# Kernel tuning notes

Measured on AMD Instinct MI355X. Metric: run time of the kernel, lower is better.

The kernel has to match this reference:

```python
import jax, jax.numpy as jnp
import numpy as np

STRIDE = 32
ANCHOR_SCALES = (16, 32, 64)
RATIOS = (0.5, 1.0, 2.0)
BASE_SIZE = 16
A = 9                    # base_anchors
PRE_NMS_TOP_N = 6000
POST_NMS_TOP_N = 1000
NMS_THRESH = 0.7
MIN_SIZE = 16.0


def _base_anchors():
    w = h = float(BASE_SIZE)
    cx = cy = (BASE_SIZE - 1) * 0.5
    out = []
    for r in RATIOS:
        ws = np.round(np.sqrt(w * h / r))
        hs = np.round(ws * r)
        for s in ANCHOR_SCALES:
            W_, H_ = ws * s, hs * s
            out.append([cx - 0.5 * (W_ - 1), cy - 0.5 * (H_ - 1),
                        cx + 0.5 * (W_ - 1), cy + 0.5 * (H_ - 1)])
    return np.asarray(out, dtype=np.float32)  # [9,4]


def _conv(x, w, b, padding):
    y = jax.lax.conv_general_dilated(x, w, (1, 1), padding,
                                     dimension_numbers=('NCHW', 'OIHW', 'NCHW'))
    return y + b[None, :, None, None]


def reference(features, rpn_w, rpn_b, cls_w, cls_b, box_w, box_b, image_height, image_width):
    H, W = features.shape[2], features.shape[3]
    x = jax.nn.relu(_conv(features, rpn_w, rpn_b, 'SAME'))
    cls_score = _conv(x, cls_w, cls_b, 'VALID')           # [1,2A,H,W]
    cls_prob = jax.nn.softmax(cls_score, axis=1)           # nn.Softmax2d: softmax over all 2A channels
    bbox_pred = _conv(x, box_w, box_b, 'VALID')            # [1,4A,H,W]

    scores = cls_prob[0, A:].transpose(1, 2, 0).reshape(-1)       # fg scores [H*W*A]
    deltas = bbox_pred[0].transpose(1, 2, 0).reshape(-1, 4)        # [H*W*A,4]

    base = jnp.asarray(_base_anchors())
    sx = jnp.arange(W, dtype=jnp.float32) * STRIDE
    sy = jnp.arange(H, dtype=jnp.float32) * STRIDE
    sxx, syy = jnp.meshgrid(sx, sy)                                # [H,W]
    shifts = jnp.stack([sxx, syy, sxx, syy], axis=-1).reshape(-1, 4)
    anchors = (shifts[:, None, :] + base[None, :, :]).reshape(-1, 4)

    # bbox_transform_inv decode
    wa = anchors[:, 2] - anchors[:, 0] + 1.0
    ha = anchors[:, 3] - anchors[:, 1] + 1.0
    cxa = anchors[:, 0] + 0.5 * (wa - 1.0)
    cya = anchors[:, 1] + 0.5 * (ha - 1.0)
    cx = deltas[:, 0] * wa + cxa
    cy = deltas[:, 1] * ha + cya
    pw = wa * jnp.exp(deltas[:, 2])
    ph = ha * jnp.exp(deltas[:, 3])
    x1 = jnp.clip(cx - 0.5 * pw, 0.0, image_width - 1.0)
    y1 = jnp.clip(cy - 0.5 * ph, 0.0, image_height - 1.0)
    x2 = jnp.clip(cx + 0.5 * pw, 0.0, image_width - 1.0)
    y2 = jnp.clip(cy + 0.5 * ph, 0.0, image_height - 1.0)
    boxes = jnp.stack([x1, y1, x2, y2], axis=-1)

    valid0 = ((x2 - x1 + 1.0) >= MIN_SIZE) & ((y2 - y1 + 1.0) >= MIN_SIZE)
    scores = jnp.where(valid0, scores, -jnp.inf)

    top_scores, top_idx = jax.lax.top_k(scores, PRE_NMS_TOP_N)
    tb = boxes[top_idx]                                             # [P,4]
    tx1, ty1, tx2, ty2 = tb[:, 0], tb[:, 1], tb[:, 2], tb[:, 3]
    areas = (tx2 - tx1 + 1.0) * (ty2 - ty1 + 1.0)
    xx1 = jnp.maximum(tx1[:, None], tx1[None, :])
    yy1 = jnp.maximum(ty1[:, None], ty1[None, :])
    xx2 = jnp.minimum(tx2[:, None], tx2[None, :])
    yy2 = jnp.minimum(ty2[:, None], ty2[None, :])
    inter = jnp.maximum(xx2 - xx1 + 1.0, 0.0) * jnp.maximum(yy2 - yy1 + 1.0, 0.0)
    iou = inter / (areas[:, None] + areas[None, :] - inter)         # [P,P]

    def step(state, _):
        alive, = (state,) if not isinstance(state, tuple) else (None,)
        return state, None

    def nms_step(state, _):
        alive, sel_list = state
        s = jnp.where(alive, top_scores, -jnp.inf)
        j = jnp.argmax(s)
        ok = s[j] > -jnp.inf
        alive = alive & (jnp.take(iou, j, axis=0) <= NMS_THRESH)    # suppresses j too (iou=1)
        return (alive, sel_list), (j.astype(jnp.int32), ok)

    alive0 = jnp.isfinite(top_scores)
    (_, _), (sel, selv) = jax.lax.scan(nms_step, (alive0, 0),
                                       jnp.arange(POST_NMS_TOP_N), length=POST_NMS_TOP_N)

    out_boxes = tb[sel] * selv[:, None].astype(tb.dtype)            # zero-pad invalid slots
    rois = jnp.concatenate([jnp.zeros((POST_NMS_TOP_N, 1), tb.dtype), out_boxes], axis=1)
    return rois                                                     # [POST_NMS_TOP_N, 5]


def setup_inputs() -> dict:
    key = jax.random.key(0)
    ks = jax.random.split(key, 4)
    features = jax.random.normal(ks[0], (1, 256, 128, 128), dtype=jnp.float32)
    rpn_w = 0.01 * jax.random.normal(ks[1], (256, 256, 3, 3), dtype=jnp.float32)
    rpn_b = jnp.zeros((256,), jnp.float32)
    cls_w = 0.01 * jax.random.normal(ks[2], (18, 256, 1, 1), dtype=jnp.float32)
    cls_b = jnp.zeros((18,), jnp.float32)
    box_w = 0.01 * jax.random.normal(ks[3], (36, 256, 1, 1), dtype=jnp.float32)
    box_b = jnp.zeros((36,), jnp.float32)
    return {'features': features, 'rpn_w': rpn_w, 'rpn_b': rpn_b,
            'cls_w': cls_w, 'cls_b': cls_b, 'box_w': box_w, 'box_b': box_b,
            'image_height': 4096, 'image_width': 4096}
```

## Files before the change

kernel.cpp:

```cpp
#include <hip/hip_runtime.h>
#include <stdint.h>
#include <math.h>

typedef unsigned long long u64;
typedef unsigned int u32;
typedef float float4a __attribute__((ext_vector_type(4), aligned(4)));

static const size_t OFF_CTL   = 0;
static const size_t OFF_HIST  = 1024;
static const size_t OFF_DOTS  = 1049600;
static const size_t OFF_WCV   = 4588544;
static const size_t OFF_XD    = 6947840;
static const size_t OFF_BOX   = 23725056;
static const size_t OFF_KEYS  = 26084352;
static const size_t OFF_CKEY  = 27264000;
static const size_t OFF_CIDX  = 27313152;
static const size_t OFF_TB    = 27337728;
static const size_t OFF_TSC   = 27433728;
static const size_t OFF_ALIVE = 27458048;
static const size_t OFF_MASK  = 27459072;
static const size_t OFF_FPAD  = 32067584;

__device__ __forceinline__ float exp_xla(float x) {
    float m = floorf(__fmaf_rn(x, 1.44269504088896341f, 0.5f));
    float r = __fmaf_rn(m, -0.693359375f, x);
    r = __fmaf_rn(m, 2.12194440e-4f, r);
    float r2 = r * r;
    float p = 1.9875691500e-4f;
    p = __fmaf_rn(p, r, 1.3981999507e-3f);
    p = __fmaf_rn(p, r, 8.3334519073e-3f);
    p = __fmaf_rn(p, r, 4.1665795894e-2f);
    p = __fmaf_rn(p, r, 1.6666665459e-1f);
    p = __fmaf_rn(p, r, 5.0000001201e-1f);
    p = __fmaf_rn(p, r2, r);
    p = __fadd_rn(p, 1.0f);
    int mi = (int)m;
    return p * __int_as_float((mi + 127) << 23);
}

__device__ __forceinline__ void gload_lds16(const void* g, void* l) {
    __builtin_amdgcn_global_load_lds(
        (const __attribute__((address_space(1))) void*)g,
        (__attribute__((address_space(3))) void*)l, 16, 0, 0);
}

__global__ void prep_wcv(const float* __restrict__ rpn_w, float* __restrict__ wcv) {
    int t = blockIdx.x * 256 + threadIdx.x;
    if (t >= 589824) return;
    int tap = t / 65536, rem = t % 65536, ic = rem / 256, oc = rem % 256;
    wcv[t] = rpn_w[oc * 2304 + ic * 9 + tap];
}

__global__ void prep_pad(const float* __restrict__ feat, float* __restrict__ featP) {
    int t = blockIdx.x * 256 + threadIdx.x;
    if (t >= 256 * 130 * 132) return;
    int ic = t / 17160, rem = t % 17160, y = rem / 132, x = rem % 132;
    int sy = y - 1, sx = x - 1;
    float v = 0.f;
    if (sy >= 0 && sy < 128 && sx >= 0 && sx < 128)
        v = feat[ic * 16384 + sy * 128 + sx];
    featP[t] = v;
}

__global__ __launch_bounds__(256, 2) void conv3x3(const float* __restrict__ featP,
                                                  const float* __restrict__ wcv,
                                                  const float* __restrict__ rpn_b,
                                                  float* __restrict__ xd) {
    __shared__ float sW[8192];
    const int band = blockIdx.x & 7;
    const int slot = blockIdx.x >> 3;
    const int tx = slot & 7, ocb = slot >> 3;
    const int oc0 = ocb * 32;
    const int tid = threadIdx.x;
    const int wid = tid >> 6;
    const int lane = tid & 63;
    const int py = lane >> 2, px0 = (lane & 3) * 4;
    const int gy = band * 16 + py, gx0 = tx * 16 + px0;
    const int ocB = oc0 + wid * 8;
    float acc[4][8];
#pragma unroll
    for (int p = 0; p < 4; ++p)
#pragma unroll
        for (int o = 0; o < 8; ++o) acc[p][o] = 0.f;
#pragma unroll
    for (int tap = 0; tap < 9; ++tap) {
        __syncthreads();
        for (int idx = tid; idx < 8192; idx += 256)
            sW[idx] = wcv[tap * 65536 + (idx >> 5) * 256 + oc0 + (idx & 31)];
        __syncthreads();
        const float* fp = featP + (size_t)(gy + tap / 3) * 132 + (gx0 + tap % 3);
        const float* wl = sW + wid * 8;
#pragma unroll 4
        for (int ic = 0; ic < 256; ++ic) {
            float4a fA = *(const float4a*)(fp + (size_t)ic * 17160);
            float4a w0 = *(const float4a*)(wl + ic * 32);
            float4a w1 = *(const float4a*)(wl + ic * 32 + 4);
#pragma unroll
            for (int p = 0; p < 4; ++p) {
#pragma unroll
                for (int o = 0; o < 4; ++o)
                    acc[p][o] = __fmaf_rn(fA[p], w0[o], acc[p][o]);
#pragma unroll
                for (int o = 0; o < 4; ++o)
                    acc[p][4 + o] = __fmaf_rn(fA[p], w1[o], acc[p][4 + o]);
            }
        }
    }
#pragma unroll
    for (int p = 0; p < 4; ++p) {
        float* op = xd + (size_t)(gy * 128 + gx0 + p) * 256 + ocB;
#pragma unroll
        for (int o = 0; o < 8; ++o) {
            float v = __fadd_rn(acc[p][o], rpn_b[ocB + o]);
            op[o] = v > 0.f ? v : 0.f;
        }
    }
}

__global__ __launch_bounds__(256, 1) void heads_seq(const float* __restrict__ xd,
                                                    const float* __restrict__ cls_w,
                                                    const float* __restrict__ box_w,
                                                    float* __restrict__ dots) {
    __shared__ float sX[4][260];
    const int tid = threadIdx.x;
    const int pix0 = blockIdx.x * 4;
    for (int idx = tid; idx < 1024; idx += 256)
        sX[idx >> 8][idx & 255] = xd[(size_t)(pix0 + (idx >> 8)) * 256 + (idx & 255)];
    __syncthreads();
    if (tid < 216) {
        const int pl = tid / 54, o = tid % 54;
        const float* wr = (o < 18) ? (cls_w + o * 256) : (box_w + (o - 18) * 256);
        const float4* x4 = (const float4*)&sX[pl][0];
        const float4* w4 = (const float4*)wr;
        float acc = 0.f;
        for (int q = 0; q < 64; ++q) {
            float4 xv = x4[q];
            float4 wv = w4[q];
            acc = __fmaf_rn(xv.x, wv.x, acc);
            acc = __fmaf_rn(xv.y, wv.y, acc);
            acc = __fmaf_rn(xv.z, wv.z, acc);
            acc = __fmaf_rn(xv.w, wv.w, acc);
        }
        dots[(size_t)(pix0 + pl) * 54 + o] = acc;
    }
}

__global__ __launch_bounds__(256, 1) void decode(const float* __restrict__ dots,
                                                 const float* __restrict__ cls_b,
                                                 const float* __restrict__ box_b,
                                                 float4* __restrict__ boxes,
                                                 u64* __restrict__ keys) {
    const int pix = blockIdx.x * 256 + threadIdx.x;
    if (pix >= 16384) return;
    const float* dt = dots + (size_t)pix * 54;
    float d[54];
#pragma unroll
    for (int i = 0; i < 54; ++i)
        d[i] = __fadd_rn(dt[i], (i < 18 ? cls_b[i] : box_b[i - 18]));
    float m = d[0];
#pragma unroll
    for (int i = 1; i < 18; ++i) m = fmaxf(m, d[i]);
    float e[18];
#pragma unroll
    for (int i = 0; i < 18; ++i) e[i] = exp_xla(__fsub_rn(d[i], m));
    float s = e[0];
#pragma unroll
    for (int i = 1; i < 18; ++i) s = __fadd_rn(s, e[i]);
    const int y = pix >> 7, x = pix & 127;
    const float shx = (float)(x * 32), shy = (float)(y * 32);
    const float AW[9] = {368.f, 736.f, 1472.f, 256.f, 512.f, 1024.f, 176.f, 352.f, 704.f};
    const float AH[9] = {192.f, 384.f, 768.f, 256.f, 512.f, 1024.f, 352.f, 704.f, 1408.f};
#pragma unroll
    for (int a = 0; a < 9; ++a) {
        float score = e[9 + a] / s;
        float wa = AW[a], ha = AH[a];
        float cxa = __fadd_rn(shx, 7.5f), cya = __fadd_rn(shy, 7.5f);
        float dx = d[18 + 4 * a], dyy = d[19 + 4 * a];
        float dw = d[20 + 4 * a], dh = d[21 + 4 * a];
        float cx = __fadd_rn(__fmul_rn(dx, wa), cxa);
        float cy = __fadd_rn(__fmul_rn(dyy, ha), cya);
        float pw = __fmul_rn(wa, exp_xla(dw));
        float ph = __fmul_rn(ha, exp_xla(dh));
        float hx = __fmul_rn(0.5f, pw), hy = __fmul_rn(0.5f, ph);
        float x1 = fminf(fmaxf(__fsub_rn(cx, hx), 0.f), 4095.f);
        float y1 = fminf(fmaxf(__fsub_rn(cy, hy), 0.f), 4095.f);
        float x2 = fminf(fmaxf(__fadd_rn(cx, hx), 0.f), 4095.f);
        float y2 = fminf(fmaxf(__fadd_rn(cy, hy), 0.f), 4095.f);
        float vw = __fadd_rn(__fsub_rn(x2, x1), 1.0f);
        float vh = __fadd_rn(__fsub_rn(y2, y1), 1.0f);
        bool valid = (vw >= 16.0f) && (vh >= 16.0f);
        int i = pix * 9 + a;
        boxes[i] = make_float4(x1, y1, x2, y2);
        u64 k;
        if (valid) {
            u32 b = __float_as_uint(score);
            k = ((u64)(u32)~(b | 0x80000000u) << 32) | (u32)i;
        } else {
            k = (0xFFFFFFFFULL << 32) | (u32)i;
        }
        keys[i] = k;
    }
}

__global__ __launch_bounds__(256) void hist8(const u64* __restrict__ keys,
                                             u32* __restrict__ ghist,
                                             const u64* __restrict__ pfx, int pass) {
    __shared__ u32 lh[256];
    lh[threadIdx.x] = 0;
    __syncthreads();
    const u64 pref = *pfx;
    const int shift = 56 - 8 * pass;
    for (int i = blockIdx.x * 256 + threadIdx.x; i < 147456; i += 64 * 256) {
        u64 k = keys[i];
        bool match = (pass == 0) || ((k >> (shift + 8)) == pref);
        if (match) atomicAdd(&lh[(u32)(k >> shift) & 0xFFu], 1u);
    }
    __syncthreads();
    if (lh[threadIdx.x]) atomicAdd(&ghist[threadIdx.x], lh[threadIdx.x]);
}

__global__ __launch_bounds__(256) void scan8(const u32* __restrict__ ghist,
                                             u64* pfx, u32* tgt, int pass) {
    __shared__ u32 h[256];
    __shared__ u32 incl[256];
    const int t = threadIdx.x;
    u32 target = (pass == 0) ? 6000u : *tgt;
    u64 p0 = (pass == 0) ? 0ULL : *pfx;
    h[t] = ghist[t];
    incl[t] = h[t];
    __syncthreads();
    for (int off = 1; off < 256; off <<= 1) {
        u32 v = (t >= off) ? incl[t - off] : 0u;
        __syncthreads();
        incl[t] += v;
        __syncthreads();
    }
    u32 before = incl[t] - h[t];
    if (before < target && target <= incl[t]) {
        *pfx = (p0 << 8) | (u64)t;
        *tgt = target - before;
    }
}

__global__ void compact(const u64* __restrict__ keys, const u64* __restrict__ kstar,
                        u32* count, u64* __restrict__ ckey, u32* __restrict__ cidx) {
    int i = blockIdx.x * 256 + threadIdx.x;
    if (i >= 147456) return;
    u64 k = keys[i];
    if (k <= *kstar) {
        u32 pos = atomicAdd(count, 1u);
        if (pos < 6144) { ckey[pos] = k; cidx[pos] = (u32)(k & 0xFFFFFFFFu); }
    }
}

__global__ __launch_bounds__(256) void rank_scatter(const u64* __restrict__ ckey,
                                                    const u32* __restrict__ cidx,
                                                    const u32* __restrict__ count,
                                                    const float4* __restrict__ boxes,
                                                    float4* __restrict__ tb,
                                                    float* __restrict__ tsc) {
    __shared__ u64 LK[6144];
    int N = (int)*count; if (N > 6144) N = 6144;
    for (int i = threadIdx.x; i < N; i += 256) LK[i] = ckey[i];
    __syncthreads();
    int e = blockIdx.x * 256 + threadIdx.x;
    if (e >= N) return;
    u64 myK = LK[e];
    u32 myI = cidx[e];
    int rank = 0;
    for (int c = 0; c < N; ++c) rank += (LK[c] < myK);
    if (rank < 6000) {
        tb[rank] = boxes[myI];
        u32 hi = (u32)(myK >> 32);
        tsc[rank] = (hi == 0xFFFFFFFFu) ? -__builtin_inff()
                                        : __uint_as_float(~hi & 0x7FFFFFFFu);
    }
}

__global__ void alive_init(const float* __restrict__ tsc, u64* __restrict__ alive0) {
    int r = blockIdx.x * 256 + threadIdx.x;
    bool a = false;
    if (r < 6000) a = tsc[r] > -__builtin_inff();
    u64 b = __ballot(a);
    if ((threadIdx.x & 63) == 0) alive0[r >> 6] = b;
}

__global__ __launch_bounds__(256) void nms_mask(const float4* __restrict__ tb,
                                                u64* __restrict__ mask) {
    int tid = blockIdx.x * 256 + threadIdx.x;
    if (tid >= 6000 * 94) return;
    int j = tid / 94, w = tid % 94;
    float4 bj = tb[j];
    float arJ = __fmul_rn(__fadd_rn(__fsub_rn(bj.z, bj.x), 1.0f),
                          __fadd_rn(__fsub_rn(bj.w, bj.y), 1.0f));
    u64 m = 0;
    int base = w * 64;
#pragma unroll 4
    for (int b = 0; b < 64; ++b) {
        int i = base + b;
        if (i >= 6000) break;
        float4 bi = tb[i];
        float arI = __fmul_rn(__fadd_rn(__fsub_rn(bi.z, bi.x), 1.0f),
                              __fadd_rn(__fsub_rn(bi.w, bi.y), 1.0f));
        float xx1 = fmaxf(bj.x, bi.x), yy1 = fmaxf(bj.y, bi.y);
        float xx2 = fminf(bj.z, bi.z), yy2 = fminf(bj.w, bi.w);
        float ww = fmaxf(__fadd_rn(__fsub_rn(xx2, xx1), 1.0f), 0.0f);
        float hh = fmaxf(__fadd_rn(__fsub_rn(yy2, yy1), 1.0f), 0.0f);
        float inter = __fmul_rn(ww, hh);
        float uni = __fsub_rn(__fadd_rn(arJ, arI), inter);
        float iou = inter / uni;
        if (iou > 0.7f) m |= (1ULL << b);
    }
    mask[(size_t)j * 96 + w] = m;
}

__global__ __launch_bounds__(64, 1) void nms_seq(const u64* __restrict__ alive0,
                                                 const u64* __restrict__ mask,
                                                 const float4* __restrict__ tb,
                                                 float* __restrict__ out) {
    __shared__ __align__(16) u64 lwin[2][64 * 96];
    __shared__ u32 sel[1000];
    const int lane = threadIdx.x;
    u64 wl = alive0[lane];
    u64 wh = (lane < 30) ? alive0[64 + lane] : 0ULL;
    int base = -1000000;
    int pbase = -1;
    int cur = 0;
    int k = 0;
    for (; k < 1000; ++k) {
        int j;
        {
            u64 blo = __ballot(wl != 0ULL);
            if (blo) {
                int l = __ffsll((long long)blo) - 1;
                u32 a = __builtin_amdgcn_readlane((u32)wl, l);
                u32 b = __builtin_amdgcn_readlane((u32)(wl >> 32), l);
                u64 w = ((u64)b << 32) | (u64)a;
                j = l * 64 + __ffsll((long long)w) - 1;
            } else {
                u64 bhi = __ballot(wh != 0ULL);
                if (!bhi) break;
                int l = __ffsll((long long)bhi) - 1;
                u32 a = __builtin_amdgcn_readlane((u32)wh, l);
                u32 b = __builtin_amdgcn_readlane((u32)(wh >> 32), l);
                u64 w = ((u64)b << 32) | (u64)a;
                j = (64 + l) * 64 + __ffsll((long long)w) - 1;
            }
        }
        if (lane == 0) sel[k] = (u32)j;
        if (j >= base + 64) {
            if (pbase >= 0 && j < pbase + 64) {
                asm volatile("s_waitcnt vmcnt(0)" ::: "memory");
                cur ^= 1;
                base = pbase;
            } else {
                int js = (j > 5936) ? 5936 : j;
                asm volatile("s_waitcnt vmcnt(0)" ::: "memory");
                const char* gsrc = (const char*)mask + (size_t)js * 768 + (size_t)lane * 16;
                char* ldst = (char*)&lwin[cur][0];
#pragma unroll
                for (int i = 0; i < 48; ++i)
                    gload_lds16(gsrc + (size_t)i * 1024, ldst + i * 1024);
                base = js;
                asm volatile("s_waitcnt vmcnt(0)" ::: "memory");
            }
            pbase = -1;
            if (base + 64 < 6000) {
                int ps = (base + 64 > 5936) ? 5936 : (base + 64);
                const char* gs2 = (const char*)mask + (size_t)ps * 768 + (size_t)lane * 16;
                char* ld2 = (char*)&lwin[cur ^ 1][0];
#pragma unroll
                for (int i = 0; i < 48; ++i)
                    gload_lds16(gs2 + (size_t)i * 1024, ld2 + i * 1024);
                pbase = ps;
            }
        }
        const int s = j - base;
        u64 rl = lwin[cur][(size_t)s * 96 + lane];
        u64 rh = (lane < 30) ? lwin[cur][(size_t)s * 96 + 64 + lane] : 0ULL;
        wl &= ~rl;
        if (lane < 30) wh &= ~rh;
    }
    __syncthreads();
    for (int r = lane; r < k; r += 64) {
        int j = (int)sel[r];
        float4 bj = tb[j];
        out[r * 5 + 1] = bj.x;
        out[r * 5 + 2] = bj.y;
        out[r * 5 + 3] = bj.z;
        out[r * 5 + 4] = bj.w;
    }
}

extern "C" void kernel_launch(void* const* d_in, const int* in_sizes, int n_in,
                              void* d_out, int out_size, void* d_ws, size_t ws_size,
                              hipStream_t stream) {
    const float *feat = nullptr, *rpn_w = nullptr, *rpn_b = nullptr;
    const float *cls_w = nullptr, *cls_b = nullptr, *box_w = nullptr, *box_b = nullptr;
    for (int i = 0; i < n_in; ++i) {
        switch (in_sizes[i]) {
            case 4194304: feat  = (const float*)d_in[i]; break;
            case 589824:  rpn_w = (const float*)d_in[i]; break;
            case 256:     rpn_b = (const float*)d_in[i]; break;
            case 4608:    cls_w = (const float*)d_in[i]; break;
            case 18:      cls_b = (const float*)d_in[i]; break;
            case 9216:    box_w = (const float*)d_in[i]; break;
            case 36:      box_b = (const float*)d_in[i]; break;
            default: break;
        }
    }

    char* w = (char*)d_ws;
    u64* pfx       = (u64*)(w + OFF_CTL);
    u32* tgt       = (u32*)(w + OFF_CTL + 8);
    u32* ctlCount  = (u32*)(w + OFF_CTL + 12);
    u32* hist      = (u32*)(w + OFF_HIST);
    float* dots    = (float*)(w + OFF_DOTS);
    float* wcv     = (float*)(w + OFF_WCV);
    float* xd      = (float*)(w + OFF_XD);
    float4* boxes  = (float4*)(w + OFF_BOX);
    u64* keys      = (u64*)(w + OFF_KEYS);
    u64* ckey      = (u64*)(w + OFF_CKEY);
    u32* cidx      = (u32*)(w + OFF_CIDX);
    float4* tb     = (float4*)(w + OFF_TB);
    float* tsc     = (float*)(w + OFF_TSC);
    u64* alive0    = (u64*)(w + OFF_ALIVE);
    u64* mask      = (u64*)(w + OFF_MASK);
    float* featP   = (float*)(w + OFF_FPAD);

    hipMemsetAsync(d_ws, 0, OFF_HIST + 8 * 256 * 4, stream);
    hipMemsetAsync(d_out, 0, (size_t)out_size * sizeof(float), stream);

    prep_wcv<<<2304, 256, 0, stream>>>(rpn_w, wcv);
    prep_pad<<<17160, 256, 0, stream>>>(feat, featP);
    conv3x3<<<512, 256, 0, stream>>>(featP, wcv, rpn_b, xd);
    heads_seq<<<4096, 256, 0, stream>>>(xd, cls_w, box_w, dots);
    decode<<<64, 256, 0, stream>>>(dots, cls_b, box_b, boxes, keys);
    for (int p = 0; p < 8; ++p) {
        hist8<<<64, 256, 0, stream>>>(keys, hist + p * 256, pfx, p);
        scan8<<<1, 256, 0, stream>>>(hist + p * 256, pfx, tgt, p);
    }
    compact<<<576, 256, 0, stream>>>(keys, pfx, ctlCount, ckey, cidx);
    rank_scatter<<<24, 256, 0, stream>>>(ckey, cidx, ctlCount, boxes, tb, tsc);
    alive_init<<<24, 256, 0, stream>>>(tsc, alive0);
    nms_mask<<<2204, 256, 0, stream>>>(tb, mask);
    nms_seq<<<1, 64, 0, stream>>>(alive0, mask, tb, (float*)d_out);
}
```

Measured before the change: 912.4 us.

## Fuse histogram and scan via last-block pattern; pad NMS mask rows for vector LDS reads

Merges each radix-select histogram pass with its prefix scan into one kernel, where the last block to finish (found with an atomic counter) does the scan. This cuts eight kernel launches from the select loop. It also pads the NMS mask rows from 96 to 128 words, interleaved so each lane reads its low and high words with one 16-byte LDS load in the serial NMS loop. The cost is more mask traffic per window, the mask buffer now sharing the padded-feature region, and a reliance on threadfence ordering in the fused kernel.

```diff
diff --git a/kernel.cpp b/kernel.cpp
--- a/kernel.cpp
+++ b/kernel.cpp
@@ -5,6 +5,7 @@
 typedef unsigned long long u64;
 typedef unsigned int u32;
 typedef float float4a __attribute__((ext_vector_type(4), aligned(4)));
+typedef unsigned long long u64x2 __attribute__((ext_vector_type(2), aligned(16)));
 
 static const size_t OFF_CTL   = 0;
 static const size_t OFF_HIST  = 1024;
@@ -18,8 +19,8 @@
 static const size_t OFF_TB    = 27337728;
 static const size_t OFF_TSC   = 27433728;
 static const size_t OFF_ALIVE = 27458048;
-static const size_t OFF_MASK  = 27459072;
 static const size_t OFF_FPAD  = 32067584;
+static const size_t OFF_MASKP = OFF_FPAD;
 
 __device__ __forceinline__ float exp_xla(float x) {
     float m = floorf(__fmaf_rn(x, 1.44269504088896341f, 0.5f));
@@ -202,32 +203,39 @@
     }
 }
 
-__global__ __launch_bounds__(256) void hist8(const u64* __restrict__ keys,
-                                             u32* __restrict__ ghist,
-                                             const u64* __restrict__ pfx, int pass) {
+__global__ __launch_bounds__(256) void hist_scan(const u64* __restrict__ keys,
+                                                 u32* __restrict__ ghist,
+                                                 u64* pfx, u32* tgt,
+                                                 u32* done, int pass) {
     __shared__ u32 lh[256];
-    lh[threadIdx.x] = 0;
+    __shared__ u32 lastFlag;
+    __shared__ u32 h[256];
+    __shared__ u32 incl[256];
+    const int t = threadIdx.x;
+    lh[t] = 0;
+    if (t == 0) lastFlag = 0;
     __syncthreads();
     const u64 pref = *pfx;
+    const u32 target0 = (pass == 0) ? 6000u : *tgt;
     const int shift = 56 - 8 * pass;
-    for (int i = blockIdx.x * 256 + threadIdx.x; i < 147456; i += 64 * 256) {
+    for (int i = blockIdx.x * 256 + t; i < 147456; i += 64 * 256) {
         u64 k = keys[i];
         bool match = (pass == 0) || ((k >> (shift + 8)) == pref);
         if (match) atomicAdd(&lh[(u32)(k >> shift) & 0xFFu], 1u);
     }
     __syncthreads();
-    if (lh[threadIdx.x]) atomicAdd(&ghist[threadIdx.x], lh[threadIdx.x]);
-}
-
-__global__ __launch_bounds__(256) void scan8(const u32* __restrict__ ghist,
-                                             u64* pfx, u32* tgt, int pass) {
-    __shared__ u32 h[256];
-    __shared__ u32 incl[256];
-    const int t = threadIdx.x;
-    u32 target = (pass == 0) ? 6000u : *tgt;
-    u64 p0 = (pass == 0) ? 0ULL : *pfx;
-    h[t] = ghist[t];
-    incl[t] = h[t];
+    if (lh[t]) atomicAdd(&ghist[t], lh[t]);
+    __threadfence();
+    __syncthreads();
+    if (t == 0) {
+        u32 prev = atomicAdd(done, 1u);
+        if (prev == 63) lastFlag = 1;
+    }
+    __syncthreads();
+    if (!lastFlag) return;
+    u32 hv = atomicAdd(&ghist[t], 0u);
+    h[t] = hv;
+    incl[t] = hv;
     __syncthreads();
     for (int off = 1; off < 256; off <<= 1) {
         u32 v = (t >= off) ? incl[t - off] : 0u;
@@ -235,10 +243,11 @@
         incl[t] += v;
         __syncthreads();
     }
+    u64 p0 = (pass == 0) ? 0ULL : pref;
     u32 before = incl[t] - h[t];
-    if (before < target && target <= incl[t]) {
+    if (before < target0 && target0 <= incl[t]) {
         *pfx = (p0 << 8) | (u64)t;
-        *tgt = target - before;
+        *tgt = target0 - before;
     }
 }
 
@@ -311,14 +320,14 @@
         float iou = inter / uni;
         if (iou > 0.7f) m |= (1ULL << b);
     }
-    mask[(size_t)j * 96 + w] = m;
+    mask[(size_t)j * 128 + 2 * (w & 63) + (w >> 6)] = m;
 }
 
 __global__ __launch_bounds__(64, 1) void nms_seq(const u64* __restrict__ alive0,
                                                  const u64* __restrict__ mask,
                                                  const float4* __restrict__ tb,
                                                  float* __restrict__ out) {
-    __shared__ __align__(16) u64 lwin[2][64 * 96];
+    __shared__ __align__(16) u64 lwin[2][64 * 128];
     __shared__ u32 sel[1000];
     const int lane = threadIdx.x;
     u64 wl = alive0[lane];
@@ -356,10 +365,10 @@
             } else {
                 int js = (j > 5936) ? 5936 : j;
                 asm volatile("s_waitcnt vmcnt(0)" ::: "memory");
-                const char* gsrc = (const char*)mask + (size_t)js * 768 + (size_t)lane * 16;
+                const char* gsrc = (const char*)mask + (size_t)js * 1024 + (size_t)lane * 16;
                 char* ldst = (char*)&lwin[cur][0];
 #pragma unroll
-                for (int i = 0; i < 48; ++i)
+                for (int i = 0; i < 64; ++i)
                     gload_lds16(gsrc + (size_t)i * 1024, ldst + i * 1024);
                 base = js;
                 asm volatile("s_waitcnt vmcnt(0)" ::: "memory");
@@ -367,17 +376,18 @@
             pbase = -1;
             if (base + 64 < 6000) {
                 int ps = (base + 64 > 5936) ? 5936 : (base + 64);
-                const char* gs2 = (const char*)mask + (size_t)ps * 768 + (size_t)lane * 16;
+                const char* gs2 = (const char*)mask + (size_t)ps * 1024 + (size_t)lane * 16;
                 char* ld2 = (char*)&lwin[cur ^ 1][0];
 #pragma unroll
-                for (int i = 0; i < 48; ++i)
+                for (int i = 0; i < 64; ++i)
                     gload_lds16(gs2 + (size_t)i * 1024, ld2 + i * 1024);
                 pbase = ps;
             }
         }
         const int s = j - base;
-        u64 rl = lwin[cur][(size_t)s * 96 + lane];
-        u64 rh = (lane < 30) ? lwin[cur][(size_t)s * 96 + 64 + lane] : 0ULL;
+        u64x2 rd = *(const u64x2*)&lwin[cur][(size_t)s * 128 + 2 * lane];
+        u64 rl = rd.x;
+        u64 rh = rd.y;
         wl &= ~rl;
         if (lane < 30) wh &= ~rh;
     }
@@ -414,6 +424,7 @@
     u64* pfx       = (u64*)(w + OFF_CTL);
     u32* tgt       = (u32*)(w + OFF_CTL + 8);
     u32* ctlCount  = (u32*)(w + OFF_CTL + 12);
+    u32* done      = (u32*)(w + OFF_CTL + 16);
     u32* hist      = (u32*)(w + OFF_HIST);
     float* dots    = (float*)(w + OFF_DOTS);
     float* wcv     = (float*)(w + OFF_WCV);
@@ -425,7 +436,7 @@
     float4* tb     = (float4*)(w + OFF_TB);
     float* tsc     = (float*)(w + OFF_TSC);
     u64* alive0    = (u64*)(w + OFF_ALIVE);
-    u64* mask      = (u64*)(w + OFF_MASK);
+    u64* maskP     = (u64*)(w + OFF_MASKP);
     float* featP   = (float*)(w + OFF_FPAD);
 
     hipMemsetAsync(d_ws, 0, OFF_HIST + 8 * 256 * 4, stream);
@@ -436,13 +447,11 @@
     conv3x3<<<512, 256, 0, stream>>>(featP, wcv, rpn_b, xd);
     heads_seq<<<4096, 256, 0, stream>>>(xd, cls_w, box_w, dots);
     decode<<<64, 256, 0, stream>>>(dots, cls_b, box_b, boxes, keys);
-    for (int p = 0; p < 8; ++p) {
-        hist8<<<64, 256, 0, stream>>>(keys, hist + p * 256, pfx, p);
-        scan8<<<1, 256, 0, stream>>>(hist + p * 256, pfx, tgt, p);
-    }
+    for (int p = 0; p < 8; ++p)
+        hist_scan<<<64, 256, 0, stream>>>(keys, hist + p * 256, pfx, tgt, done + p, p);
     compact<<<576, 256, 0, stream>>>(keys, pfx, ctlCount, ckey, cidx);
     rank_scatter<<<24, 256, 0, stream>>>(ckey, cidx, ctlCount, boxes, tb, tsc);
     alive_init<<<24, 256, 0, stream>>>(tsc, alive0);
-    nms_mask<<<2204, 256, 0, stream>>>(tb, mask);
-    nms_seq<<<1, 64, 0, stream>>>(alive0, mask, tb, (float*)d_out);
-}
+    nms_mask<<<2204, 256, 0, stream>>>(tb, maskP);
+    nms_seq<<<1, 64, 0, stream>>>(alive0, maskP, tb, (float*)d_out);
+}
```

New measurement: 904.6 us. About the same (-0.9%).
